# Performance work log

Measured on AMD Instinct MI355X. Metric: run time of the kernel, lower is better.

## Reference

```python
import jax, jax.numpy as jnp
import numpy as np
from jax import lax

HEADS = 8
DIM_HEAD = 8
SCALE = DIM_HEAD ** (-0.5)
UP = 64  # nn.Upsample(scale_factor=64), nearest


def _conv_s8(x, w, b):
    # Conv2d(inner, inner, 11x11, stride 8, padding 2) + exact GELU
    y = lax.conv_general_dilated(x, w, window_strides=(8, 8),
                                 padding=((2, 2), (2, 2)),
                                 dimension_numbers=('NCHW', 'OIHW', 'NCHW'))
    return jax.nn.gelu(y + b[None, :, None, None], approximate=False)


def setup_inputs() -> dict:
    key = jax.random.key(0)
    ks = jax.random.split(key, 8)
    b, c, h, w = 2, 64, 48, 48
    inner = HEADS * DIM_HEAD  # 64
    f = jax.random.normal(ks[0], (b, c, h, w), jnp.float32)
    w_qkv = jax.random.normal(ks[1], (inner * 3, c, 1, 1), jnp.float32) * 0.05
    wq = jax.random.normal(ks[2], (inner, inner, 11, 11), jnp.float32) * 0.02
    bq = jax.random.normal(ks[3], (inner,), jnp.float32) * 0.02
    wk = jax.random.normal(ks[4], (inner, inner, 11, 11), jnp.float32) * 0.02
    bk = jax.random.normal(ks[5], (inner,), jnp.float32) * 0.02
    pos_h = jax.random.normal(ks[6], (DIM_HEAD, h), jnp.float32) * SCALE
    pos_w = jax.random.normal(ks[7], (DIM_HEAD, w), jnp.float32) * SCALE
    return {"f": f, "w_qkv": w_qkv, "wq": wq, "bq": bq, "wk": wk,
            "bk": bk, "pos_h": pos_h, "pos_w": pos_w}


def reference(f, w_qkv, wq, bq, wk, bk, pos_h, pos_w):
    b, c, h, w = f.shape
    inner = HEADS * DIM_HEAD
    # 1x1 conv to qkv
    qkv = jnp.einsum('oc,bchw->bohw', w_qkv[:, :, 0, 0], f)
    q, k, v = jnp.split(qkv, 3, axis=1)  # each [b, inner, h, w]
    # positional logits from pre-conv q
    q_full = q.reshape(b, HEADS, DIM_HEAD, h * w)
    emb = (pos_h[:, :, None] + pos_w[:, None, :]).reshape(DIM_HEAD, h * w)
    pos_logits = jnp.einsum('bhci,cj->bhij', q_full, emb)  # [b,H,hw,hw]
    # strided conv + gelu on q,k
    qd = _conv_s8(q, wq, bq)
    kd = _conv_s8(k, wk, bk)
    m = qd.shape[-1]  # downsampled side
    qd = qd.reshape(b, HEADS, DIM_HEAD, m * m) * SCALE
    kd = kd.reshape(b, HEADS, DIM_HEAD, m * m)
    vv = v.reshape(b, HEADS, DIM_HEAD, h * w)
    dots = jnp.einsum('bhci,bhcj->bhij', qd, kd)  # [b,H,m^2,m^2]
    # nearest upsample x64 on last two dims
    dots = jnp.repeat(jnp.repeat(dots, UP, axis=-2), UP, axis=-1)
    attn = jax.nn.softmax(dots + pos_logits, axis=-1)
    fmap = jnp.einsum('bhij,bhcj->bhci', attn, vv)
    return fmap.reshape(b, inner, h, w)
```

## Files before the change

### kernel.cpp

```cpp
#include <hip/hip_runtime.h>
#include <math.h>

#define HW 2304
#define O192 192
#define SCALE_F 0.35355339059327373f

typedef unsigned int u32;
typedef __attribute__((address_space(1))) const u32 gu32;
typedef __attribute__((address_space(3))) u32 lu32;
__device__ __forceinline__ void dma16(const void* g, void* l) {
  __builtin_amdgcn_global_load_lds((gu32*)g, (lu32*)l, 16, 0, 0);
}

__global__ __launch_bounds__(256) void qkv_kernel(
    const float* __restrict__ F, const float* __restrict__ W,
    float* __restrict__ QKV, float* __restrict__ V2) {
  __shared__ __align__(16) float sW[384];
  int blk = blockIdx.x;
  int idx0 = blk * 256;
  int r0 = idx0 / HW;
  int r1 = (idx0 + 255) / HW;
  int tid = threadIdx.x;
  if (tid < 192) {
    int g = tid >> 6, c = tid & 63;
    sW[tid]       = W[((r0 & 63) + g * 64) * 64 + c];
    sW[192 + tid] = W[((r1 & 63) + g * 64) * 64 + c];
  }
  __syncthreads();
  int idx = idx0 + tid;
  int p  = idx % HW;
  int r  = idx / HW;
  int o0 = r & 63;
  int b  = r >> 6;
  const float4* w4 = (const float4*)(sW + ((r == r0) ? 0 : 192));
  const float* f = F + (b * 64) * HW + p;
  float aq = 0.f, ak = 0.f, av = 0.f;
  #pragma unroll 4
  for (int c4 = 0; c4 < 16; c4++) {
    float4 wq = w4[c4];
    float4 wk = w4[16 + c4];
    float4 wv = w4[32 + c4];
    float f0 = f[(c4 * 4 + 0) * HW];
    float f1 = f[(c4 * 4 + 1) * HW];
    float f2 = f[(c4 * 4 + 2) * HW];
    float f3 = f[(c4 * 4 + 3) * HW];
    aq = fmaf(wq.x, f0, aq); ak = fmaf(wk.x, f0, ak); av = fmaf(wv.x, f0, av);
    aq = fmaf(wq.y, f1, aq); ak = fmaf(wk.y, f1, ak); av = fmaf(wv.y, f1, av);
    aq = fmaf(wq.z, f2, aq); ak = fmaf(wk.z, f2, ak); av = fmaf(wv.z, f2, av);
    aq = fmaf(wq.w, f3, aq); ak = fmaf(wk.w, f3, ak); av = fmaf(wv.w, f3, av);
  }
  float* qp = QKV + (b * HW + p) * O192;
  qp[o0]      = aq;
  qp[o0 + 64] = ak;
  V2[(((b << 3) + (o0 >> 3)) * HW + p) * 8 + (o0 & 7)] = av;
}

__global__ __launch_bounds__(256) void conv_kernel(
    const float* __restrict__ QKV, const float* __restrict__ Wq,
    const float* __restrict__ Bq, const float* __restrict__ Wk,
    const float* __restrict__ Bk, float* __restrict__ QD) {
  __shared__ float sW[7744];
  __shared__ float sRed[4 * 64 * 6];
  int blk = blockIdx.x;
  int xcd = blk & 7;
  int T = xcd >> 2, b = (xcd >> 1) & 1, s = xcd & 1;
  int idx = (blk >> 3) * 2 + s;
  int o  = idx / 6;
  int oy = idx % 6;
  const float* Wg = T ? Wk : Wq;
  for (int i = threadIdx.x; i < 7744; i += 256) sW[i] = Wg[o * 7744 + i];
  __syncthreads();
  int wv = threadIdx.x >> 6;
  int c  = threadIdx.x & 63;
  const float* base = QKV + b * (HW * O192) + T * 64 + c;
  float acc[6];
  #pragma unroll
  for (int ox = 0; ox < 6; ox++) acc[ox] = 0.f;
  for (int kyi = 0; kyi < 3; kyi++) {
    int ky = wv * 3 + kyi;
    if (ky > 10) break;
    int y = oy * 8 - 2 + ky;
    if ((unsigned)y < 48u) {
      float xrow[48];
      #pragma unroll
      for (int x = 0; x < 48; x++) xrow[x] = base[(y * 48 + x) * O192];
      #pragma unroll
      for (int kx = 0; kx < 11; kx++) {
        float wt = sW[c * 121 + ky * 11 + kx];
        #pragma unroll
        for (int ox = 0; ox < 6; ox++) {
          int x = ox * 8 - 2 + kx;
          if (x >= 0 && x < 48) acc[ox] = fmaf(xrow[x], wt, acc[ox]);
        }
      }
    }
  }
  #pragma unroll
  for (int ox = 0; ox < 6; ox++) sRed[(wv * 64 + c) * 6 + ox] = acc[ox];
  __syncthreads();
  if (threadIdx.x < 64) {
    int t = threadIdx.x;
    float r[6];
    #pragma unroll
    for (int ox = 0; ox < 6; ox++)
      r[ox] = sRed[t * 6 + ox] + sRed[(64 + t) * 6 + ox]
            + sRed[(128 + t) * 6 + ox] + sRed[(192 + t) * 6 + ox];
    #pragma unroll
    for (int off = 32; off; off >>= 1) {
      #pragma unroll
      for (int ox = 0; ox < 6; ox++) r[ox] += __shfl_down(r[ox], off, 64);
    }
    if (t == 0) {
      float bias = T ? Bk[o] : Bq[o];
      #pragma unroll
      for (int ox = 0; ox < 6; ox++) {
        float g = r[ox] + bias;
        float ge = 0.5f * g * (1.0f + erff(g * 0.70710678118654752f));
        QD[((T * 2 + b) * 64 + o) * 36 + oy * 6 + ox] = ge;
      }
    }
  }
}

#define OFF_V   0
#define OFF_EA  4608
#define OFF_PHT 5376
#define OFF_PWT 5760
#define OFF_E4  6144
#define OFF_Q   6192
#define OFF_R   6704
#define SBUF_N  11312

__global__ __launch_bounds__(512, 4) void attn_kernel(
    const float* __restrict__ QKV, const float* __restrict__ V2,
    const float* __restrict__ QD, const float* __restrict__ PH,
    const float* __restrict__ PW, float* __restrict__ out) {
  __shared__ __align__(16) float sB[SBUF_N];
  int blk = blockIdx.x;
  int bh = blk / 36;
  int S  = blk - bh * 36;
  int b = bh >> 3, h = bh & 7;
  int tid = threadIdx.x;
  int w = tid >> 6, lane = tid & 63;
  if (tid < 384) {
    sB[OFF_PHT + tid] = PH[(tid & 7) * 48 + (tid >> 3)];
    sB[OFF_PWT + tid] = PW[(tid & 7) * 48 + (tid >> 3)];
  }
  if (tid < 36) {
    float acc = 0.f;
    #pragma unroll
    for (int c8 = 0; c8 < 8; c8++) {
      float qv = QD[((0 + b) * 64 + h * 8 + c8) * 36 + S];
      float kv = QD[((2 + b) * 64 + h * 8 + c8) * 36 + tid];
      acc = fmaf(qv, kv, acc);
    }
    sB[OFF_E4 + tid] = __expf(SCALE_F * acc);
  }
  if (tid < 128) {
    *(float4*)(sB + OFF_Q + tid * 4) =
      *(const float4*)(QKV + (b * HW + S * 64 + (tid >> 1)) * O192 + h * 8 + (tid & 1) * 4);
  }
  {
    const char* src = (const char*)(V2 + (size_t)bh * (HW * 8));
    for (int m = w; m < 18; m += 8)
      dma16(src + m * 1024 + lane * 16, (char*)(sB + OFF_V) + m * 1024);
  }
  __syncthreads();
  float eB[6];
  {
    const float* qp = sB + OFF_Q + lane * 8;
    #pragma unroll
    for (int i = 0; i < 6; i++) {
      const float* pp = sB + OFF_PWT + (w * 6 + i) * 8;
      float d = qp[0]*pp[0]+qp[1]*pp[1]+qp[2]*pp[2]+qp[3]*pp[3]
              + qp[4]*pp[4]+qp[5]*pp[5]+qp[6]*pp[6]+qp[7]*pp[7];
      eB[i] = __expf(d);
    }
  }
  float acc[9];
  #pragma unroll
  for (int c = 0; c < 9; c++) acc[c] = 0.f;
  const float4* sV4 = (const float4*)(sB + OFF_V);
  for (int q = 0; q < 4; q++) {
    #pragma unroll
    for (int m = 0; m < 2; m++) {
      int flat = tid + m * 512;
      if (flat < 768) {
        int jyL = flat >> 6, ln = flat & 63;
        const float* qp = sB + OFF_Q + ln * 8;
        const float* pp = sB + OFF_PHT + (q * 12 + jyL) * 8;
        float d = qp[0]*pp[0]+qp[1]*pp[1]+qp[2]*pp[2]+qp[3]*pp[3]
                + qp[4]*pp[4]+qp[5]*pp[5]+qp[6]*pp[6]+qp[7]*pp[7];
        sB[OFF_EA + flat] = __expf(d);
      }
    }
    __syncthreads();
    for (int jyL = 0; jyL < 12; jyL++) {
      float eAk = sB[OFF_EA + jyL * 64 + lane];
      int cb = (q * 12 + jyL) * 48 + w * 6;
      int J0 = cb >> 6, J1 = (cb + 5) >> 6;
      int ib = 64 - (cb & 63);
      float e0 = sB[OFF_E4 + J0];
      float e1 = sB[OFF_E4 + J1];
      float a0 = eAk * e0, a1 = eAk * e1;
      #pragma unroll
      for (int i = 0; i < 6; i++) {
        float4 vlo = sV4[(jyL * 48 + w * 6 + i) * 2];
        float4 vhi = sV4[(jyL * 48 + w * 6 + i) * 2 + 1];
        float wgt = (i < ib ? a0 : a1) * eB[i];
        acc[0] = fmaf(wgt, vlo.x, acc[0]);
        acc[1] = fmaf(wgt, vlo.y, acc[1]);
        acc[2] = fmaf(wgt, vlo.z, acc[2]);
        acc[3] = fmaf(wgt, vlo.w, acc[3]);
        acc[4] = fmaf(wgt, vhi.x, acc[4]);
        acc[5] = fmaf(wgt, vhi.y, acc[5]);
        acc[6] = fmaf(wgt, vhi.z, acc[6]);
        acc[7] = fmaf(wgt, vhi.w, acc[7]);
        acc[8] += wgt;
      }
    }
    if (q < 3) {
      __syncthreads();
      const char* src = (const char*)(V2 + (size_t)bh * (HW * 8) + (q + 1) * 4608);
      for (int m = w; m < 18; m += 8)
        dma16(src + m * 1024 + lane * 16, (char*)(sB + OFF_V) + m * 1024);
    }
  }
  #pragma unroll
  for (int c = 0; c < 9; c++) sB[OFF_R + (w * 64 + lane) * 9 + c] = acc[c];
  __syncthreads();
  {
    int c = tid >> 6, r = tid & 63;
    float num = 0.f, z = 0.f;
    #pragma unroll
    for (int ww = 0; ww < 8; ww++) {
      num += sB[OFF_R + (ww * 64 + r) * 9 + c];
      z   += sB[OFF_R + (ww * 64 + r) * 9 + 8];
    }
    out[(b * 64 + h * 8 + c) * HW + S * 64 + r] = num / z;
  }
}

extern "C" void kernel_launch(void* const* d_in, const int* in_sizes, int n_in,
                              void* d_out, int out_size, void* d_ws, size_t ws_size,
                              hipStream_t stream) {
  const float* F    = (const float*)d_in[0];
  const float* Wqkv = (const float*)d_in[1];
  const float* Wq   = (const float*)d_in[2];
  const float* Bq   = (const float*)d_in[3];
  const float* Wk   = (const float*)d_in[4];
  const float* Bk   = (const float*)d_in[5];
  const float* PH   = (const float*)d_in[6];
  const float* PW   = (const float*)d_in[7];
  float* out = (float*)d_out;

  float* ws   = (float*)d_ws;
  float* QKV  = ws;
  float* V2   = QKV + 2 * HW * O192;
  float* QD   = V2 + 2 * 8 * HW * 8;

  qkv_kernel <<<1152, 256, 0, stream>>>(F, Wqkv, QKV, V2);
  conv_kernel<<<1536, 256, 0, stream>>>(QKV, Wq, Bq, Wk, Bk, QD);
  attn_kernel<<<576,  512, 0, stream>>>(QKV, V2, QD, PH, PW, out);
}
```

Before: 139.6 us.

## Split attention blocks to 32 query rows and read V directly from global

The attention kernel now handles 32 query rows per block instead of 64, doubling the grid to 1152 blocks. Each half-wave owns 3 key columns, so lanes are regrouped and the two halves are combined with a cross-half shuffle. V is no longer staged into LDS with async global-to-LDS copies in four phases. Each thread reads V straight from global (relying on cache), which removes the per-phase barriers and shrinks LDS to allow more resident blocks, at the cost of more global/L2 traffic and less V reuse per block.

```diff
diff --git a/kernel.cpp b/kernel.cpp
--- a/kernel.cpp
+++ b/kernel.cpp
@@ -6,11 +6,6 @@
 #define SCALE_F 0.35355339059327373f
 
 typedef unsigned int u32;
-typedef __attribute__((address_space(1))) const u32 gu32;
-typedef __attribute__((address_space(3))) u32 lu32;
-__device__ __forceinline__ void dma16(const void* g, void* l) {
-  __builtin_amdgcn_global_load_lds((gu32*)g, (lu32*)l, 16, 0, 0);
-}
 
 __global__ __launch_bounds__(256) void qkv_kernel(
     const float* __restrict__ F, const float* __restrict__ W,
@@ -122,14 +117,13 @@
   }
 }
 
-#define OFF_V   0
-#define OFF_EA  4608
-#define OFF_PHT 5376
-#define OFF_PWT 5760
-#define OFF_E4  6144
-#define OFF_Q   6192
-#define OFF_R   6704
-#define SBUF_N  11312
+#define OFF_EA  0
+#define OFF_PHT 1536
+#define OFF_PWT 1920
+#define OFF_E   2304
+#define OFF_QT  2344
+#define OFF_R   2600
+#define SBUF_N  4904
 
 __global__ __launch_bounds__(512, 4) void attn_kernel(
     const float* __restrict__ QKV, const float* __restrict__ V2,
@@ -137,107 +131,98 @@
     const float* __restrict__ PW, float* __restrict__ out) {
   __shared__ __align__(16) float sB[SBUF_N];
   int blk = blockIdx.x;
-  int bh = blk / 36;
-  int S  = blk - bh * 36;
+  int bh = blk / 72;
+  int S  = blk - bh * 72;
   int b = bh >> 3, h = bh & 7;
   int tid = threadIdx.x;
   int w = tid >> 6, lane = tid & 63;
+  int rl = lane & 31;
+  int g  = w * 2 + (lane >> 5);
   if (tid < 384) {
     sB[OFF_PHT + tid] = PH[(tid & 7) * 48 + (tid >> 3)];
     sB[OFF_PWT + tid] = PW[(tid & 7) * 48 + (tid >> 3)];
   }
   if (tid < 36) {
+    int I = S >> 1;
     float acc = 0.f;
     #pragma unroll
     for (int c8 = 0; c8 < 8; c8++) {
-      float qv = QD[((0 + b) * 64 + h * 8 + c8) * 36 + S];
+      float qv = QD[((0 + b) * 64 + h * 8 + c8) * 36 + I];
       float kv = QD[((2 + b) * 64 + h * 8 + c8) * 36 + tid];
       acc = fmaf(qv, kv, acc);
     }
-    sB[OFF_E4 + tid] = __expf(SCALE_F * acc);
-  }
-  if (tid < 128) {
-    *(float4*)(sB + OFF_Q + tid * 4) =
-      *(const float4*)(QKV + (b * HW + S * 64 + (tid >> 1)) * O192 + h * 8 + (tid & 1) * 4);
-  }
-  {
-    const char* src = (const char*)(V2 + (size_t)bh * (HW * 8));
-    for (int m = w; m < 18; m += 8)
-      dma16(src + m * 1024 + lane * 16, (char*)(sB + OFF_V) + m * 1024);
-  }
-  __syncthreads();
-  float eB[6];
-  {
-    const float* qp = sB + OFF_Q + lane * 8;
-    #pragma unroll
-    for (int i = 0; i < 6; i++) {
-      const float* pp = sB + OFF_PWT + (w * 6 + i) * 8;
-      float d = qp[0]*pp[0]+qp[1]*pp[1]+qp[2]*pp[2]+qp[3]*pp[3]
-              + qp[4]*pp[4]+qp[5]*pp[5]+qp[6]*pp[6]+qp[7]*pp[7];
-      eB[i] = __expf(d);
-    }
-  }
+    sB[OFF_E + tid] = __expf(SCALE_F * acc);
+  }
+  if (tid < 256) {
+    int row = tid >> 3, c = tid & 7;
+    sB[OFF_QT + c * 32 + row] =
+      QKV[(b * HW + S * 32 + row) * O192 + h * 8 + c];
+  }
+  __syncthreads();
+  #pragma unroll
+  for (int m = 0; m < 3; m++) {
+    int flat = tid + m * 512;
+    int jy = flat >> 5, r = flat & 31;
+    const float* pp = sB + OFF_PHT + jy * 8;
+    float d = 0.f;
+    #pragma unroll
+    for (int j = 0; j < 8; j++) d = fmaf(sB[OFF_QT + j * 32 + r], pp[j], d);
+    sB[OFF_EA + flat] = __expf(d);
+  }
+  float eB[3];
+  #pragma unroll
+  for (int i = 0; i < 3; i++) {
+    const float* pp = sB + OFF_PWT + (g * 3 + i) * 8;
+    float d = 0.f;
+    #pragma unroll
+    for (int j = 0; j < 8; j++) d = fmaf(sB[OFF_QT + j * 32 + rl], pp[j], d);
+    eB[i] = __expf(d);
+  }
+  __syncthreads();
   float acc[9];
   #pragma unroll
   for (int c = 0; c < 9; c++) acc[c] = 0.f;
-  const float4* sV4 = (const float4*)(sB + OFF_V);
-  for (int q = 0; q < 4; q++) {
-    #pragma unroll
-    for (int m = 0; m < 2; m++) {
-      int flat = tid + m * 512;
-      if (flat < 768) {
-        int jyL = flat >> 6, ln = flat & 63;
-        const float* qp = sB + OFF_Q + ln * 8;
-        const float* pp = sB + OFF_PHT + (q * 12 + jyL) * 8;
-        float d = qp[0]*pp[0]+qp[1]*pp[1]+qp[2]*pp[2]+qp[3]*pp[3]
-                + qp[4]*pp[4]+qp[5]*pp[5]+qp[6]*pp[6]+qp[7]*pp[7];
-        sB[OFF_EA + flat] = __expf(d);
-      }
-    }
-    __syncthreads();
-    for (int jyL = 0; jyL < 12; jyL++) {
-      float eAk = sB[OFF_EA + jyL * 64 + lane];
-      int cb = (q * 12 + jyL) * 48 + w * 6;
-      int J0 = cb >> 6, J1 = (cb + 5) >> 6;
-      int ib = 64 - (cb & 63);
-      float e0 = sB[OFF_E4 + J0];
-      float e1 = sB[OFF_E4 + J1];
-      float a0 = eAk * e0, a1 = eAk * e1;
-      #pragma unroll
-      for (int i = 0; i < 6; i++) {
-        float4 vlo = sV4[(jyL * 48 + w * 6 + i) * 2];
-        float4 vhi = sV4[(jyL * 48 + w * 6 + i) * 2 + 1];
-        float wgt = (i < ib ? a0 : a1) * eB[i];
-        acc[0] = fmaf(wgt, vlo.x, acc[0]);
-        acc[1] = fmaf(wgt, vlo.y, acc[1]);
-        acc[2] = fmaf(wgt, vlo.z, acc[2]);
-        acc[3] = fmaf(wgt, vlo.w, acc[3]);
-        acc[4] = fmaf(wgt, vhi.x, acc[4]);
-        acc[5] = fmaf(wgt, vhi.y, acc[5]);
-        acc[6] = fmaf(wgt, vhi.z, acc[6]);
-        acc[7] = fmaf(wgt, vhi.w, acc[7]);
-        acc[8] += wgt;
-      }
-    }
-    if (q < 3) {
-      __syncthreads();
-      const char* src = (const char*)(V2 + (size_t)bh * (HW * 8) + (q + 1) * 4608);
-      for (int m = w; m < 18; m += 8)
-        dma16(src + m * 1024 + lane * 16, (char*)(sB + OFF_V) + m * 1024);
-    }
-  }
-  #pragma unroll
-  for (int c = 0; c < 9; c++) sB[OFF_R + (w * 64 + lane) * 9 + c] = acc[c];
-  __syncthreads();
-  {
-    int c = tid >> 6, r = tid & 63;
+  const float4* v4 = (const float4*)(V2 + (size_t)bh * (HW * 8));
+  for (int jy = 0; jy < 48; jy++) {
+    float eAk = sB[OFF_EA + jy * 32 + rl];
+    int cb = jy * 48 + g * 3;
+    int J0 = cb >> 6, J1 = (cb + 2) >> 6;
+    int ib = 64 - (cb & 63);
+    float e0 = sB[OFF_E + J0];
+    float e1 = sB[OFF_E + J1];
+    float a0 = eAk * e0, a1 = eAk * e1;
+    #pragma unroll
+    for (int i = 0; i < 3; i++) {
+      float4 vlo = v4[(cb + i) * 2];
+      float4 vhi = v4[(cb + i) * 2 + 1];
+      float wgt = (i < ib ? a0 : a1) * eB[i];
+      acc[0] = fmaf(wgt, vlo.x, acc[0]);
+      acc[1] = fmaf(wgt, vlo.y, acc[1]);
+      acc[2] = fmaf(wgt, vlo.z, acc[2]);
+      acc[3] = fmaf(wgt, vlo.w, acc[3]);
+      acc[4] = fmaf(wgt, vhi.x, acc[4]);
+      acc[5] = fmaf(wgt, vhi.y, acc[5]);
+      acc[6] = fmaf(wgt, vhi.z, acc[6]);
+      acc[7] = fmaf(wgt, vhi.w, acc[7]);
+      acc[8] += wgt;
+    }
+  }
+  #pragma unroll
+  for (int c = 0; c < 9; c++) acc[c] += __shfl_xor(acc[c], 32, 64);
+  if (lane < 32) {
+    #pragma unroll
+    for (int c = 0; c < 9; c++) sB[OFF_R + (w * 32 + rl) * 9 + c] = acc[c];
+  }
+  __syncthreads();
+  if (tid < 256) {
+    int r = tid & 31, c = tid >> 5;
     float num = 0.f, z = 0.f;
     #pragma unroll
     for (int ww = 0; ww < 8; ww++) {
-      num += sB[OFF_R + (ww * 64 + r) * 9 + c];
-      z   += sB[OFF_R + (ww * 64 + r) * 9 + 8];
-    }
-    out[(b * 64 + h * 8 + c) * HW + S * 64 + r] = num / z;
+      num += sB[OFF_R + (ww * 32 + r) * 9 + c];
+      z   += sB[OFF_R + (ww * 32 + r) * 9 + 8];
+    }
+    out[(b * 64 + h * 8 + c) * HW + S * 32 + r] = num / z;
   }
 }
 
@@ -261,5 +246,5 @@
 
   qkv_kernel <<<1152, 256, 0, stream>>>(F, Wqkv, QKV, V2);
   conv_kernel<<<1536, 256, 0, stream>>>(QKV, Wq, Bq, Wk, Bk, QD);
-  attn_kernel<<<576,  512, 0, stream>>>(QKV, V2, QD, PH, PW, out);
-}
+  attn_kernel<<<1152, 512, 0, stream>>>(QKV, V2, QD, PH, PW, out);
+}
```

Measured after the change: 184.2 us. 1.32x slower.
